# Optimization experiments

Measured on AMD Instinct MI355X. Metric: run time of the kernel, lower is better.

## Reference

```python
import jax, jax.numpy as jnp
import numpy as np

OFR = 2.0      # offset_range_factor
WSIZE = 8      # window_size
SPLIT = 1      # split_size


def _grid_sample(img, grid):
    # torch.nn.functional.grid_sample: bilinear, align_corners=True, padding_mode='zeros'
    # img: (B,C,H,W); grid: (B,Gh,Gw,2) with (x,y) in [-1,1]
    B, C, H, W = img.shape
    gx = (grid[..., 0] + 1.0) * 0.5 * (W - 1)
    gy = (grid[..., 1] + 1.0) * 0.5 * (H - 1)
    x0 = jnp.floor(gx)
    y0 = jnp.floor(gy)
    wx1 = gx - x0
    wy1 = gy - y0
    imgf = img.reshape(B, C, H * W)

    def corner(yc, xc, wgt):
        valid = (xc >= 0) & (xc <= W - 1) & (yc >= 0) & (yc <= H - 1)
        idx = (jnp.clip(yc, 0, H - 1) * W + jnp.clip(xc, 0, W - 1)).astype(jnp.int32)
        g = jnp.take_along_axis(imgf, idx.reshape(B, 1, -1), axis=2)  # (B,C,N)
        return g * (wgt * valid).reshape(B, 1, -1)

    out = (corner(y0, x0, (1 - wy1) * (1 - wx1)) + corner(y0, x0 + 1, (1 - wy1) * wx1)
           + corner(y0 + 1, x0, wy1 * (1 - wx1)) + corner(y0 + 1, x0 + 1, wy1 * wx1))
    return out.reshape(B, C, *grid.shape[1:-1])


def _win_attn(xqv, dh, dw):
    # 'b (qv c) (h dh) (w dw) -> qv (b h w) (dh dw) c' ; dot attention ; inverse rearrange
    B, cc, H, W = xqv.shape
    c = cc // 2
    t = xqv.reshape(B, 2, c, H // dh, dh, W // dw, dw)
    t = t.transpose(1, 0, 3, 5, 4, 6, 2).reshape(2, -1, dh * dw, c)
    q, v = t[0], t[1]
    atn = jax.nn.softmax(q @ jnp.swapaxes(q, -1, -2), axis=-1)
    o = atn @ v  # (nw, dh*dw, c)
    o = o.reshape(B, H // dh, W // dw, dh, dw, c).transpose(0, 5, 1, 3, 2, 4).reshape(B, c, H, W)
    return o


def setup_inputs() -> dict:
    key = jax.random.key(0)
    ks = jax.random.split(key, 16)
    C, B, H, W = 48, 2, 64, 64
    rn = lambda k, s, sc=0.05: (jax.random.normal(k, s) * sc).astype(jnp.float32)
    return {
        'x': jax.random.normal(ks[0], (B, C, H, W), jnp.float32),
        'Wq': rn(ks[1], (C, C)), 'bq': rn(ks[2], (C,)),
        'off_dw_w': rn(ks[3], (C, 1, 3, 3)), 'off_dw_b': rn(ks[4], (C,)),
        'off_ln_g': jnp.ones((C,), jnp.float32), 'off_ln_b': jnp.zeros((C,), jnp.float32),
        'off_pw_w': rn(ks[5], (2, C)),
        'Wk': rn(ks[6], (C, C)), 'bk': rn(ks[7], (C,)),
        'Wv': rn(ks[8], (C, C)), 'bv': rn(ks[9], (C,)),
        'inp_w': rn(ks[10], (2 * C, C)), 'inp_b': rn(ks[11], (2 * C,)),
        'bn_g': jnp.ones((2 * C,), jnp.float32), 'bn_b': jnp.zeros((2 * C,), jnp.float32),
        'bn_mean': jnp.zeros((2 * C,), jnp.float32), 'bn_var': jnp.ones((2 * C,), jnp.float32),
        'pout_w': rn(ks[12], (C, C)), 'pout_b': rn(ks[13], (C,)),
        'rpe': rn(ks[14], (1, 191, 191), 0.01),  # 96*2-1
    }


def reference(x, Wq, bq, off_dw_w, off_dw_b, off_ln_g, off_ln_b, off_pw_w, Wk, bk, Wv, bv,
              inp_w, inp_b, bn_g, bn_b, bn_mean, bn_var, pout_w, pout_b, rpe):
    B, C, h, w = x.shape
    scale = C ** (-0.5)
    c1 = lambda t, W_, b_=None: jnp.einsum('oc,bchw->bohw', W_, t) + (0.0 if b_ is None else b_[None, :, None, None])
    q = c1(x, Wq, bq)
    # conv_offset: depthwise 3x3 -> LayerNorm over channels -> GELU -> 1x1 to 2 ch (no bias)
    t = jax.lax.conv_general_dilated(q, off_dw_w, (1, 1), ((1, 1), (1, 1)),
                                     dimension_numbers=('NCHW', 'OIHW', 'NCHW'),
                                     feature_group_count=C) + off_dw_b[None, :, None, None]
    mu = t.mean(1, keepdims=True)
    var = ((t - mu) ** 2).mean(1, keepdims=True)
    t = (t - mu) * jax.lax.rsqrt(var + 1e-5) * off_ln_g[None, :, None, None] + off_ln_b[None, :, None, None]
    t = jax.nn.gelu(t, approximate=False)
    offset = c1(t, off_pw_w)  # (B,2,h,w), channel 0 = y, 1 = x
    n = h * w
    orange = jnp.array([1.0 / (h - 1), 1.0 / (w - 1)], jnp.float32).reshape(1, 2, 1, 1)
    offset = jnp.tanh(offset) * orange * OFR
    offset = offset.transpose(0, 2, 3, 1)  # (B,h,w,2) (y,x)
    ry = jnp.linspace(0.5, h - 0.5, h) / (h - 1) * 2.0 - 1.0
    rx = jnp.linspace(0.5, w - 0.5, w) / (w - 1) * 2.0 - 1.0
    ref = jnp.stack(jnp.meshgrid(ry, rx, indexing='ij'), -1)[None]
    pos = offset + ref  # (B,h,w,2) (y,x)
    x_sampled = _grid_sample(x, pos[..., ::-1]).reshape(B, C, n)
    # project_inp: 1x1 conv -> BatchNorm2d (eval mode)
    x2 = c1(x, inp_w, inp_b)
    x2 = (x2 - bn_mean[None, :, None, None]) * jax.lax.rsqrt(bn_var + 1e-5)[None, :, None, None] \
         * bn_g[None, :, None, None] + bn_b[None, :, None, None]
    s = 2 * C // 3
    xs0, xs1, xs2 = x2[:, :s], x2[:, s:2 * s], x2[:, 2 * s:]
    # deformable global attention
    qf = q.reshape(B, C, n)
    k = jnp.einsum('oc,bcn->bon', Wk, x_sampled) + bk[None, :, None]
    v = jnp.einsum('oc,bcn->bon', Wv, x_sampled) + bv[None, :, None]
    attn = jnp.einsum('bcm,bcn->bmn', qf, k) * scale
    gy = jnp.arange(h, dtype=jnp.float32) / (h - 1) * 2.0 - 1.0
    gx = jnp.arange(w, dtype=jnp.float32) / (w - 1) * 2.0 - 1.0
    qg = jnp.stack(jnp.meshgrid(gy, gx, indexing='ij'), -1).reshape(n, 2)
    disp = (qg[None, :, None, :] - pos.reshape(B, n, 2)[:, None, :, :]) * 0.5  # (B,m,n,2) (y,x)
    rpe_img = jnp.broadcast_to(rpe[None], (B,) + rpe.shape)  # (B,1,191,191)
    attn_bias = _grid_sample(rpe_img, disp[..., ::-1]).reshape(B, n, n)
    attn = jax.nn.softmax(attn + attn_bias, axis=2)
    out_dat = jnp.einsum('bmn,bcn->bcm', attn, v).reshape(B, C, h, w)
    # windowed / column / row local attention (shifts=0)
    out = jnp.concatenate([_win_attn(xs0, WSIZE, WSIZE),
                           _win_attn(xs1, h, SPLIT),
                           _win_attn(xs2, SPLIT, w)], axis=1)
    out = c1(out, pout_w, pout_b)
    return out * 0.5 + out_dat * 0.5
```

## Files before the change

kernel.cpp:

```cpp
#include <hip/hip_runtime.h>
#include <hip/hip_bf16.h>
#include <math.h>

#define Bsz 2
#define Cch 48
#define Hh 64
#define Ww 64
#define Nn 4096

typedef __bf16 bf16;
typedef __attribute__((ext_vector_type(8))) __bf16 bf16x8;
typedef __attribute__((ext_vector_type(4))) float f32x4;

__global__ void k_conv1x1(const float* __restrict__ in, const float* __restrict__ Wt,
                          const float* __restrict__ bias, float* __restrict__ qnc,
                          bf16* __restrict__ qbf){
  int chunk = blockIdx.x & 15;
  int o = (blockIdx.x >> 4) % Cch;
  int b = blockIdx.x / (16 * Cch);
  int p = chunk * 256 + threadIdx.x;
  float acc = bias[o];
  const float* ip = in + (b * Cch) * Nn + p;
  const float* wp = Wt + o * Cch;
  #pragma unroll
  for (int c = 0; c < Cch; c++) acc += wp[c] * ip[c * Nn];
  qnc[((size_t)(b * Nn + p)) * 48 + o] = acc;
  size_t qb = ((size_t)(b * Nn + p)) * 64;
  qbf[qb + o] = (bf16)acc;
  if (o < 16) qbf[qb + 48 + o] = (bf16)0.f;
}

__global__ __launch_bounds__(256) void k_offset_pos(const float* __restrict__ qnc,
                             const float* __restrict__ dww,
                             const float* __restrict__ dwb, const float* __restrict__ lng,
                             const float* __restrict__ lnb, const float* __restrict__ pww,
                             float* __restrict__ pos){
  int wv = threadIdx.x >> 6, lane = threadIdx.x & 63;
  int idx = blockIdx.x * 4 + wv;
  int b = idx >> 12;
  int p = idx & (Nn - 1);
  int y = p >> 6, x = p & 63;
  int c = lane;
  float t = 0.f;
  if (c < 48){
    t = dwb[c];
    #pragma unroll
    for (int ky = -1; ky <= 1; ky++){
      int yy = y + ky;
      if (yy < 0 || yy >= Hh) continue;
      #pragma unroll
      for (int kx = -1; kx <= 1; kx++){
        int xx = x + kx;
        if (xx < 0 || xx >= Ww) continue;
        t = fmaf(qnc[((size_t)(b * Nn + yy * Ww + xx)) * 48 + c],
                 dww[c * 9 + (ky + 1) * 3 + (kx + 1)], t);
      }
    }
  }
  float s = t;
  #pragma unroll
  for (int m = 1; m < 64; m <<= 1) s += __shfl_xor(s, m);
  float mean = s * (1.f / 48.f);
  float d = (c < 48) ? (t - mean) : 0.f;
  float v = d * d;
  #pragma unroll
  for (int m = 1; m < 64; m <<= 1) v += __shfl_xor(v, m);
  float rstd = rsqrtf(v * (1.f / 48.f) + 1e-5f);
  float p0 = 0.f, p1 = 0.f;
  if (c < 48){
    float u = (t - mean) * rstd * lng[c] + lnb[c];
    u = 0.5f * u * (1.f + erff(u * 0.70710678118654752f));
    p0 = pww[c] * u;
    p1 = pww[48 + c] * u;
  }
  #pragma unroll
  for (int m = 1; m < 64; m <<= 1){ p0 += __shfl_xor(p0, m); p1 += __shfl_xor(p1, m); }
  if (lane == 0){
    float posy = tanhf(p0) * (2.f / 63.f) + ((0.5f + (float)y) * (2.f / 63.f) - 1.f);
    float posx = tanhf(p1) * (2.f / 63.f) + ((0.5f + (float)x) * (2.f / 63.f) - 1.f);
    pos[idx * 2 + 0] = posy;
    pos[idx * 2 + 1] = posx;
  }
}

__global__ __launch_bounds__(512) void k_samplekv(const float* __restrict__ x,
                           const float* __restrict__ pos,
                           const float* __restrict__ Wk, const float* __restrict__ bk,
                           const float* __restrict__ Wv, const float* __restrict__ bv,
                           bf16* __restrict__ kk_bf, bf16* __restrict__ vt_bf,
                           float2* __restrict__ axay){
  __shared__ float wkt[48][49];
  __shared__ float wvt[48][49];
  __shared__ float rowb[8][48];
  int tid = threadIdx.x;
  for (int f = tid; f < 2304; f += 512){
    int o = f / 48, c = f - o * 48;
    wkt[c][o] = Wk[f];
    wvt[c][o] = Wv[f];
  }
  __syncthreads();
  int wv = tid >> 6, lane = tid & 63;
  int idx = blockIdx.x * 8 + wv;
  int b = idx >> 12;
  int n = idx & (Nn - 1);
  float py = pos[idx * 2], px = pos[idx * 2 + 1];
  if (lane == 0) axay[idx] = make_float2(95.f - 47.5f * py, 95.f - 47.5f * px);
  float gx = (px + 1.f) * 0.5f * 63.f;
  float gy = (py + 1.f) * 0.5f * 63.f;
  float x0f = floorf(gx), y0f = floorf(gy);
  float wx = gx - x0f, wy = gy - y0f;
  int x0 = (int)x0f, y0 = (int)y0f, x1 = x0 + 1, y1 = y0 + 1;
  float w00 = (1.f - wy) * (1.f - wx), w01 = (1.f - wy) * wx;
  float w10 = wy * (1.f - wx),         w11 = wy * wx;
  bool vx0 = (x0 >= 0) && (x0 < Ww), vx1 = (x1 >= 0) && (x1 < Ww);
  bool vy0 = (y0 >= 0) && (y0 < Hh), vy1 = (y1 >= 0) && (y1 < Hh);
  if (!(vx0 && vy0)) w00 = 0.f;
  if (!(vx1 && vy0)) w01 = 0.f;
  if (!(vx0 && vy1)) w10 = 0.f;
  if (!(vx1 && vy1)) w11 = 0.f;
  int cx0 = min(max(x0, 0), Ww - 1), cx1 = min(max(x1, 0), Ww - 1);
  int cy0 = min(max(y0, 0), Hh - 1), cy1 = min(max(y1, 0), Hh - 1);
  int i00 = cy0 * Ww + cx0, i01 = cy0 * Ww + cx1;
  int i10 = cy1 * Ww + cx0, i11 = cy1 * Ww + cx1;
  int c = lane;
  if (c < 48){
    const float* xc = x + ((size_t)(b * Cch + c)) * Nn;
    rowb[wv][c] = w00 * xc[i00] + w01 * xc[i01] + w10 * xc[i10] + w11 * xc[i11];
  }
  int o = lane;
  if (o < 48){
    float ka = bk[o], va = bv[o];
    #pragma unroll
    for (int cc = 0; cc < 48; cc++){
      float r = rowb[wv][cc];
      ka = fmaf(wkt[cc][o], r, ka);
      va = fmaf(wvt[cc][o], r, va);
    }
    kk_bf[(size_t)idx * 64 + o] = (bf16)ka;
    vt_bf[((size_t)(b * Cch + o)) * Nn + n] = (bf16)va;
  }
  if (o < 16) kk_bf[(size_t)idx * 64 + 48 + o] = (bf16)0.f;
}

__global__ __launch_bounds__(256, 4) void k_attn(const bf16* __restrict__ q_bf,
                                              const bf16* __restrict__ kk_bf,
                                              const bf16* __restrict__ vt_bf,
                                              const float2* __restrict__ axay,
                                              const float* __restrict__ rpe,
                                              float* __restrict__ o_part,
                                              float* __restrict__ s_part){
  __shared__ __align__(16) float g[128][26];
  __shared__ float axs[128], wy0s[128], wy1s[128];
  __shared__ int xlos[128], r0s[128], r1s[128];
  __shared__ __align__(16) bf16 ps[16][136];

  const int tid = threadIdx.x;
  const int b  = blockIdx.x >> 9;
  const int kp = (blockIdx.x >> 8) & 1;
  const int m0 = (blockIdx.x & 255) * 16;
  const int wid = tid >> 6, lane = tid & 63;
  const int q16 = lane >> 4, l16 = lane & 15;
  const int wn0 = wid * 32;

  const bf16* qb = q_bf + ((size_t)(b * Nn + m0 + l16)) * 64;
  bf16x8 qf0 = *(const bf16x8*)(qb + q16 * 8);
  bf16x8 qf1 = *(const bf16x8*)(qb + 32 + q16 * 8);

  const float qgy = (float)(m0 >> 6) * (2.f / 63.f) - 1.f;
  const float byq = 47.5f * qgy;
  const float scale = 0.14433756729740643f;
  const float bx0 = 47.5f * ((float)(m0 & 63) * (2.f / 63.f) - 1.f);
  float bxr[4];
  #pragma unroll
  for (int r = 0; r < 4; r++){
    int mcol = (m0 & 63) + q16 * 4 + r;
    bxr[r] = 47.5f * ((float)mcol * (2.f / 63.f) - 1.f);
  }

  f32x4 oacc[3];
  #pragma unroll
  for (int ct = 0; ct < 3; ct++) oacc[ct] = (f32x4){0.f, 0.f, 0.f, 0.f};
  float s_runw[4] = {0.f, 0.f, 0.f, 0.f};

  for (int chk = 0; chk < 16; chk++){
    const int n0 = kp * 2048 + chk * 128;
    if (lane < 32){
      int n = wn0 + lane;
      float2 aa = axay[(size_t)b * Nn + n0 + n];
      float gyr = aa.x + byq;
      float y0f = floorf(gyr);
      float wy = gyr - y0f;
      int y0 = (int)y0f, y1 = y0 + 1;
      wy0s[n] = ((unsigned)y0 < 191u) ? (1.f - wy) : 0.f;
      wy1s[n] = ((unsigned)y1 < 191u) ? wy : 0.f;
      r0s[n] = min(max(y0, 0), 190) * 191;
      r1s[n] = min(max(y1, 0), 190) * 191;
      axs[n] = aa.y;
      xlos[n] = (int)floorf(aa.y + bx0);
    }
    {
      int s = lane >> 5, jj = lane & 31;
      if (jj < 26){
        #pragma unroll
        for (int it = 0; it < 16; it++){
          int n = wn0 + it * 2 + s;
          int cx = min(max(xlos[n] + jj, 0), 190);
          g[n][jj] = wy0s[n] * rpe[r0s[n] + cx] + wy1s[n] * rpe[r1s[n] + cx];
        }
      }
    }
    f32x4 s0 = (f32x4){0.f, 0.f, 0.f, 0.f};
    f32x4 s1 = (f32x4){0.f, 0.f, 0.f, 0.f};
    {
      const bf16* kg = kk_bf + (size_t)(b * Nn + n0 + wn0 + l16) * 64;
      bf16x8 b00 = *(const bf16x8*)(kg + q16 * 8);
      bf16x8 b01 = *(const bf16x8*)(kg + 32 + q16 * 8);
      bf16x8 b10 = *(const bf16x8*)(kg + 16 * 64 + q16 * 8);
      bf16x8 b11 = *(const bf16x8*)(kg + 16 * 64 + 32 + q16 * 8);
      s0 = __builtin_amdgcn_mfma_f32_16x16x32_bf16(qf0, b00, s0, 0, 0, 0);
      s0 = __builtin_amdgcn_mfma_f32_16x16x32_bf16(qf1, b01, s0, 0, 0, 0);
      s1 = __builtin_amdgcn_mfma_f32_16x16x32_bf16(qf0, b10, s1, 0, 0, 0);
      s1 = __builtin_amdgcn_mfma_f32_16x16x32_bf16(qf1, b11, s1, 0, 0, 0);
    }
    float rs[4] = {0.f, 0.f, 0.f, 0.f};
    #pragma unroll
    for (int nt = 0; nt < 2; nt++){
      int nl = wn0 + nt * 16 + l16;
      float ax = axs[nl];
      int xb = xlos[nl];
      f32x4 sv = nt ? s1 : s0;
      #pragma unroll
      for (int r = 0; r < 4; r++){
        float gxr = ax + bxr[r];
        float x0f = floorf(gxr);
        float wx = gxr - x0f;
        int x0 = (int)x0f;
        float wx0 = ((unsigned)x0 < 191u) ? (1.f - wx) : 0.f;
        float wx1 = ((unsigned)(x0 + 1) < 191u) ? wx : 0.f;
        int j0 = min(max(x0 - xb, 0), 24);
        float bias = wx0 * g[nl][j0] + wx1 * g[nl][j0 + 1];
        float e = __expf(fmaf(sv[r], scale, bias));
        rs[r] += e;
        ps[q16 * 4 + r][nl] = (bf16)e;
      }
    }
    #pragma unroll
    for (int r = 0; r < 4; r++){
      float v = rs[r];
      #pragma unroll
      for (int msk = 1; msk < 16; msk <<= 1) v += __shfl_xor(v, msk);
      s_runw[r] += v;
    }
    {
      bf16x8 pa = *(const bf16x8*)&ps[l16][wn0 + q16 * 8];
      const bf16* vgb = vt_bf + (size_t)(b * Cch + l16) * Nn + n0 + wn0 + q16 * 8;
      #pragma unroll
      for (int ct = 0; ct < 3; ct++){
        bf16x8 vb = *(const bf16x8*)(vgb + (size_t)(ct * 16) * Nn);
        oacc[ct] = __builtin_amdgcn_mfma_f32_16x16x32_bf16(pa, vb, oacc[ct], 0, 0, 0);
      }
    }
  }
  __syncthreads();
  float* ored = (float*)g;
  float* sred = axs;
  #pragma unroll
  for (int ct = 0; ct < 3; ct++)
    #pragma unroll
    for (int r = 0; r < 4; r++)
      ored[(wid * 16 + q16 * 4 + r) * 48 + ct * 16 + l16] = oacc[ct][r];
  if (l16 == 0){
    #pragma unroll
    for (int r = 0; r < 4; r++) sred[wid * 16 + q16 * 4 + r] = s_runw[r];
  }
  __syncthreads();
  size_t obase = ((size_t)(b * 2 + kp) * Cch) * Nn;
  #pragma unroll
  for (int e = 0; e < 3; e++){
    int idx = tid + e * 256;
    int c = idx >> 4, mm = idx & 15;
    float v = ored[mm * 48 + c] + ored[(16 + mm) * 48 + c]
            + ored[(32 + mm) * 48 + c] + ored[(48 + mm) * 48 + c];
    o_part[obase + (size_t)c * Nn + m0 + mm] = v;
  }
  if (tid < 16)
    s_part[(size_t)(b * 2 + kp) * Nn + m0 + tid] =
        sred[tid] + sred[16 + tid] + sred[32 + tid] + sred[48 + tid];
}

__global__ __launch_bounds__(256) void k_win(const float* __restrict__ x,
                                             const float* __restrict__ iw,
                                             const float* __restrict__ ib,
                                             const float* __restrict__ bng,
                                             const float* __restrict__ bnb,
                                             const float* __restrict__ bnm,
                                             const float* __restrict__ bnv,
                                             float* __restrict__ wout){
  __shared__ __align__(16) bf16 xs[64][72];
  __shared__ __align__(16) bf16 wtt[32][72];
  __shared__ __align__(16) bf16 qs[64][72];
  __shared__ __align__(16) bf16 vst[16][72];
  __shared__ __align__(16) bf16 psw[64][72];
  __shared__ float bnsc[32], bnsh[32];
  int s = blockIdx.x >> 7;
  int r7 = blockIdx.x & 127;
  int b = r7 >> 6, wi = r7 & 63;
  int tid = threadIdx.x;
  int wid = tid >> 6, lane = tid & 63;
  int q16 = lane >> 4, l16 = lane & 15;
  for (int f = tid; f < 64 * 48; f += 256){
    int t = f & 63, c = f >> 6;
    int p = (s == 0) ? (((wi >> 3) * 8 + (t >> 3)) * 64 + (wi & 7) * 8 + (t & 7))
          : (s == 1) ? (t * 64 + wi) : (wi * 64 + t);
    xs[t][c] = (bf16)x[((size_t)(b * 48 + c)) * Nn + p];
  }
  for (int f = tid; f < 64 * 16; f += 256){
    int t = f >> 4, j = f & 15;
    xs[t][48 + j] = (bf16)0.f;
    qs[t][16 + j] = (bf16)0.f;
  }
  for (int f = tid; f < 32 * 64; f += 256){
    int o = f >> 6, c = f & 63;
    wtt[o][c] = (c < 48) ? (bf16)iw[(s * 32 + o) * 48 + c] : (bf16)0.f;
  }
  if (tid < 32){
    int ch = s * 32 + tid;
    float sc = bng[ch] * rsqrtf(bnv[ch] + 1e-5f);
    bnsc[tid] = sc;
    bnsh[tid] = (ib[ch] - bnm[ch]) * sc + bnb[ch];
  }
  __syncthreads();
  {
    bf16x8 a0 = *(const bf16x8*)&xs[wid * 16 + l16][q16 * 8];
    bf16x8 a1 = *(const bf16x8*)&xs[wid * 16 + l16][32 + q16 * 8];
    #pragma unroll
    for (int nt = 0; nt < 2; nt++){
      bf16x8 b0 = *(const bf16x8*)&wtt[nt * 16 + l16][q16 * 8];
      bf16x8 b1 = *(const bf16x8*)&wtt[nt * 16 + l16][32 + q16 * 8];
      f32x4 acc = (f32x4){0.f, 0.f, 0.f, 0.f};
      acc = __builtin_amdgcn_mfma_f32_16x16x32_bf16(a0, b0, acc, 0, 0, 0);
      acc = __builtin_amdgcn_mfma_f32_16x16x32_bf16(a1, b1, acc, 0, 0, 0);
      float scv = bnsc[nt * 16 + l16], shv = bnsh[nt * 16 + l16];
      #pragma unroll
      for (int r = 0; r < 4; r++){
        float v = fmaf(acc[r], scv, shv);
        int tok = wid * 16 + q16 * 4 + r;
        if (nt == 0) qs[tok][l16] = (bf16)v;
        else         vst[l16][tok] = (bf16)v;
      }
    }
  }
  __syncthreads();
  f32x4 sreg[4];
  {
    bf16x8 aq = *(const bf16x8*)&qs[wid * 16 + l16][q16 * 8];
    #pragma unroll
    for (int nt = 0; nt < 4; nt++){
      bf16x8 bq = *(const bf16x8*)&qs[nt * 16 + l16][q16 * 8];
      f32x4 acc = (f32x4){0.f, 0.f, 0.f, 0.f};
      sreg[nt] = __builtin_amdgcn_mfma_f32_16x16x32_bf16(aq, bq, acc, 0, 0, 0);
    }
  }
  float rinv[4];
  #pragma unroll
  for (int r = 0; r < 4; r++){
    float mx = fmaxf(fmaxf(sreg[0][r], sreg[1][r]), fmaxf(sreg[2][r], sreg[3][r]));
    #pragma unroll
    for (int msk = 1; msk < 16; msk <<= 1) mx = fmaxf(mx, __shfl_xor(mx, msk));
    float sum = 0.f;
    #pragma unroll
    for (int nt = 0; nt < 4; nt++){
      float e = __expf(sreg[nt][r] - mx);
      sum += e;
      psw[wid * 16 + q16 * 4 + r][nt * 16 + l16] = (bf16)e;
    }
    #pragma unroll
    for (int msk = 1; msk < 16; msk <<= 1) sum += __shfl_xor(sum, msk);
    rinv[r] = 1.f / sum;
  }
  f32x4 oac = (f32x4){0.f, 0.f, 0.f, 0.f};
  {
    bf16x8 pa0 = *(const bf16x8*)&psw[wid * 16 + l16][q16 * 8];
    bf16x8 pa1 = *(const bf16x8*)&psw[wid * 16 + l16][32 + q16 * 8];
    bf16x8 vb0 = *(const bf16x8*)&vst[l16][q16 * 8];
    bf16x8 vb1 = *(const bf16x8*)&vst[l16][32 + q16 * 8];
    oac = __builtin_amdgcn_mfma_f32_16x16x32_bf16(pa0, vb0, oac, 0, 0, 0);
    oac = __builtin_amdgcn_mfma_f32_16x16x32_bf16(pa1, vb1, oac, 0, 0, 0);
  }
  #pragma unroll
  for (int r = 0; r < 4; r++){
    int tok = wid * 16 + q16 * 4 + r;
    int p = (s == 0) ? (((wi >> 3) * 8 + (tok >> 3)) * 64 + (wi & 7) * 8 + (tok & 7))
          : (s == 1) ? (tok * 64 + wi) : (wi * 64 + tok);
    wout[((size_t)(b * 48 + s * 16 + l16)) * Nn + p] = oac[r] * rinv[r];
  }
}

__global__ void k_final(const float* __restrict__ win, const float* __restrict__ pw,
                        const float* __restrict__ pb, const float* __restrict__ o_part,
                        const float* __restrict__ s_part, float* __restrict__ out){
  int chunk = blockIdx.x & 15;
  int o = (blockIdx.x >> 4) % Cch;
  int b = blockIdx.x / (16 * Cch);
  int p = chunk * 256 + threadIdx.x;
  float acc = pb[o];
  const float* ip = win + (b * Cch) * Nn + p;
  const float* wp = pw + o * Cch;
  #pragma unroll
  for (int c = 0; c < Cch; c++) acc += wp[c] * ip[c * Nn];
  float sden = s_part[(size_t)(b * 2) * Nn + p] + s_part[(size_t)(b * 2 + 1) * Nn + p];
  float odv = (o_part[((size_t)(b * 2) * Cch + o) * Nn + p]
             + o_part[((size_t)(b * 2 + 1) * Cch + o) * Nn + p]) / sden;
  out[(b * Cch + o) * Nn + p] = 0.5f * acc + 0.5f * odv;
}

extern "C" void kernel_launch(void* const* d_in, const int* in_sizes, int n_in,
                              void* d_out, int out_size, void* d_ws, size_t ws_size,
                              hipStream_t stream){
  const float* x   = (const float*)d_in[0];
  const float* Wq  = (const float*)d_in[1];
  const float* bq  = (const float*)d_in[2];
  const float* dww = (const float*)d_in[3];
  const float* dwb = (const float*)d_in[4];
  const float* lng = (const float*)d_in[5];
  const float* lnb = (const float*)d_in[6];
  const float* pww = (const float*)d_in[7];
  const float* Wk  = (const float*)d_in[8];
  const float* bk  = (const float*)d_in[9];
  const float* Wv  = (const float*)d_in[10];
  const float* bv  = (const float*)d_in[11];
  const float* iw  = (const float*)d_in[12];
  const float* ib  = (const float*)d_in[13];
  const float* bng = (const float*)d_in[14];
  const float* bnb = (const float*)d_in[15];
  const float* bnm = (const float*)d_in[16];
  const float* bnv = (const float*)d_in[17];
  const float* pw  = (const float*)d_in[18];
  const float* pb  = (const float*)d_in[19];
  const float* rpe = (const float*)d_in[20];

  float*  ws     = (float*)d_ws;
  float*  qnc    = ws;
  float*  o_part = ws;
  float*  pos    = ws + 786432;
  float2* axay   = (float2*)(ws + 802816);
  float*  wout   = ws + 819200;
  bf16*   q_bf   = (bf16*)(ws + 1212416);
  bf16*   kk_bf  = (bf16*)(ws + 1474560);
  bf16*   vt_bf  = (bf16*)(ws + 1736704);
  float*  s_part = ws + 1933312;
  float*  out    = (float*)d_out;

  k_conv1x1   <<<Bsz * Cch * 16, 256, 0, stream>>>(x, Wq, bq, qnc, q_bf);
  k_offset_pos<<<(Bsz * Nn) / 4, 256, 0, stream>>>(qnc, dww, dwb, lng, lnb, pww, pos);
  k_samplekv  <<<(Bsz * Nn) / 8, 512, 0, stream>>>(x, pos, Wk, bk, Wv, bv,
                                                   kk_bf, vt_bf, axay);
  k_attn      <<<Bsz * 512, 256, 0, stream>>>(q_bf, kk_bf, vt_bf, axay, rpe,
                                              o_part, s_part);
  k_win       <<<384, 256, 0, stream>>>(x, iw, ib, bng, bnb, bnm, bnv, wout);
  k_final     <<<Bsz * Cch * 16, 256, 0, stream>>>(wout, pw, pb, o_part,
                                                   s_part, out);
}
```

Before: 206.4 us.

## Fuse global deformable attention and window attention into one launch, simplify bias sampling

Merges the deformable-attention kernel and the local window-attention kernel into a single launch: the first 1024 blocks do global attention and the remaining 384 do window attention, sharing one overlaid shared-memory buffer. It also bakes the x-boundary zeroing into the cached rpe rows so the inner bilinear bias becomes a single lerp, defers the per-row sum reduction to after the loop, and raises the launch-bounds occupancy hint from 4 to 5. The aim is to remove a launch and the tail gap between the two kernels, and to cut ALU work in the hot loop. The higher occupancy target may force register spills, and the unclamped j0 index relies on the g row covering every offset that occurs.

Result: faster. 199.6 us (-3.3%).

```diff
diff --git a/kernel.cpp b/kernel.cpp
--- a/kernel.cpp
+++ b/kernel.cpp
@@ -142,257 +142,262 @@
   if (o < 16) kk_bf[(size_t)idx * 64 + 48 + o] = (bf16)0.f;
 }
 
-__global__ __launch_bounds__(256, 4) void k_attn(const bf16* __restrict__ q_bf,
+__global__ __launch_bounds__(256, 5) void k_attn_win(const bf16* __restrict__ q_bf,
                                               const bf16* __restrict__ kk_bf,
                                               const bf16* __restrict__ vt_bf,
                                               const float2* __restrict__ axay,
                                               const float* __restrict__ rpe,
                                               float* __restrict__ o_part,
-                                              float* __restrict__ s_part){
-  __shared__ __align__(16) float g[128][26];
-  __shared__ float axs[128], wy0s[128], wy1s[128];
-  __shared__ int xlos[128], r0s[128], r1s[128];
-  __shared__ __align__(16) bf16 ps[16][136];
-
+                                              float* __restrict__ s_part,
+                                              const float* __restrict__ x,
+                                              const float* __restrict__ iw,
+                                              const float* __restrict__ ib,
+                                              const float* __restrict__ bng,
+                                              const float* __restrict__ bnb,
+                                              const float* __restrict__ bnm,
+                                              const float* __restrict__ bnv,
+                                              float* __restrict__ wout){
+  __shared__ __align__(16) char smem[25600];
   const int tid = threadIdx.x;
-  const int b  = blockIdx.x >> 9;
-  const int kp = (blockIdx.x >> 8) & 1;
-  const int m0 = (blockIdx.x & 255) * 16;
   const int wid = tid >> 6, lane = tid & 63;
   const int q16 = lane >> 4, l16 = lane & 15;
-  const int wn0 = wid * 32;
-
-  const bf16* qb = q_bf + ((size_t)(b * Nn + m0 + l16)) * 64;
-  bf16x8 qf0 = *(const bf16x8*)(qb + q16 * 8);
-  bf16x8 qf1 = *(const bf16x8*)(qb + 32 + q16 * 8);
-
-  const float qgy = (float)(m0 >> 6) * (2.f / 63.f) - 1.f;
-  const float byq = 47.5f * qgy;
-  const float scale = 0.14433756729740643f;
-  const float bx0 = 47.5f * ((float)(m0 & 63) * (2.f / 63.f) - 1.f);
-  float bxr[4];
-  #pragma unroll
-  for (int r = 0; r < 4; r++){
-    int mcol = (m0 & 63) + q16 * 4 + r;
-    bxr[r] = 47.5f * ((float)mcol * (2.f / 63.f) - 1.f);
-  }
-
-  f32x4 oacc[3];
-  #pragma unroll
-  for (int ct = 0; ct < 3; ct++) oacc[ct] = (f32x4){0.f, 0.f, 0.f, 0.f};
-  float s_runw[4] = {0.f, 0.f, 0.f, 0.f};
-
-  for (int chk = 0; chk < 16; chk++){
-    const int n0 = kp * 2048 + chk * 128;
-    if (lane < 32){
-      int n = wn0 + lane;
-      float2 aa = axay[(size_t)b * Nn + n0 + n];
-      float gyr = aa.x + byq;
-      float y0f = floorf(gyr);
-      float wy = gyr - y0f;
-      int y0 = (int)y0f, y1 = y0 + 1;
-      wy0s[n] = ((unsigned)y0 < 191u) ? (1.f - wy) : 0.f;
-      wy1s[n] = ((unsigned)y1 < 191u) ? wy : 0.f;
-      r0s[n] = min(max(y0, 0), 190) * 191;
-      r1s[n] = min(max(y1, 0), 190) * 191;
-      axs[n] = aa.y;
-      xlos[n] = (int)floorf(aa.y + bx0);
-    }
+
+  if (blockIdx.x < 1024){
+    float (*g)[26] = (float(*)[26])smem;
+    float* axs  = (float*)(smem + 13312);
+    int*   xlos = (int*)  (smem + 13824);
+    float* wy0s = (float*)(smem + 14336);
+    float* wy1s = (float*)(smem + 14848);
+    int*   r0s  = (int*)  (smem + 15360);
+    int*   r1s  = (int*)  (smem + 15872);
+    bf16 (*ps)[136] = (bf16(*)[136])(smem + 16384);
+
+    const int b  = blockIdx.x >> 9;
+    const int kp = (blockIdx.x >> 8) & 1;
+    const int m0 = (blockIdx.x & 255) * 16;
+    const int wn0 = wid * 32;
+
+    const bf16* qb = q_bf + ((size_t)(b * Nn + m0 + l16)) * 64;
+    bf16x8 qf0 = *(const bf16x8*)(qb + q16 * 8);
+    bf16x8 qf1 = *(const bf16x8*)(qb + 32 + q16 * 8);
+
+    const float qgy = (float)(m0 >> 6) * (2.f / 63.f) - 1.f;
+    const float byq = 47.5f * qgy;
+    const float scale = 0.14433756729740643f;
+    const float bx0 = 47.5f * ((float)(m0 & 63) * (2.f / 63.f) - 1.f);
+    float bxr[4];
+    #pragma unroll
+    for (int r = 0; r < 4; r++){
+      int mcol = (m0 & 63) + q16 * 4 + r;
+      bxr[r] = 47.5f * ((float)mcol * (2.f / 63.f) - 1.f);
+    }
+
+    f32x4 oacc[3];
+    #pragma unroll
+    for (int ct = 0; ct < 3; ct++) oacc[ct] = (f32x4){0.f, 0.f, 0.f, 0.f};
+    float s_runw[4] = {0.f, 0.f, 0.f, 0.f};
+
+    for (int chk = 0; chk < 16; chk++){
+      const int n0 = kp * 2048 + chk * 128;
+      if (lane < 32){
+        int n = wn0 + lane;
+        float2 aa = axay[(size_t)b * Nn + n0 + n];
+        float gyr = aa.x + byq;
+        float y0f = floorf(gyr);
+        float wy = gyr - y0f;
+        int y0 = (int)y0f, y1 = y0 + 1;
+        wy0s[n] = ((unsigned)y0 < 191u) ? (1.f - wy) : 0.f;
+        wy1s[n] = ((unsigned)y1 < 191u) ? wy : 0.f;
+        r0s[n] = min(max(y0, 0), 190) * 191;
+        r1s[n] = min(max(y1, 0), 190) * 191;
+        axs[n] = aa.y;
+        xlos[n] = (int)floorf(aa.y + bx0);
+      }
+      {
+        int s = lane >> 5, jj = lane & 31;
+        if (jj < 26){
+          #pragma unroll
+          for (int it = 0; it < 16; it++){
+            int n = wn0 + it * 2 + s;
+            int xg = xlos[n] + jj;
+            int cx = min(max(xg, 0), 190);
+            float val = wy0s[n] * rpe[r0s[n] + cx] + wy1s[n] * rpe[r1s[n] + cx];
+            g[n][jj] = ((unsigned)xg < 191u) ? val : 0.f;
+          }
+        }
+      }
+      f32x4 s0 = (f32x4){0.f, 0.f, 0.f, 0.f};
+      f32x4 s1 = (f32x4){0.f, 0.f, 0.f, 0.f};
+      {
+        const bf16* kg = kk_bf + (size_t)(b * Nn + n0 + wn0 + l16) * 64;
+        bf16x8 b00 = *(const bf16x8*)(kg + q16 * 8);
+        bf16x8 b01 = *(const bf16x8*)(kg + 32 + q16 * 8);
+        bf16x8 b10 = *(const bf16x8*)(kg + 16 * 64 + q16 * 8);
+        bf16x8 b11 = *(const bf16x8*)(kg + 16 * 64 + 32 + q16 * 8);
+        s0 = __builtin_amdgcn_mfma_f32_16x16x32_bf16(qf0, b00, s0, 0, 0, 0);
+        s0 = __builtin_amdgcn_mfma_f32_16x16x32_bf16(qf1, b01, s0, 0, 0, 0);
+        s1 = __builtin_amdgcn_mfma_f32_16x16x32_bf16(qf0, b10, s1, 0, 0, 0);
+        s1 = __builtin_amdgcn_mfma_f32_16x16x32_bf16(qf1, b11, s1, 0, 0, 0);
+      }
+      #pragma unroll
+      for (int nt = 0; nt < 2; nt++){
+        int nl = wn0 + nt * 16 + l16;
+        float ax = axs[nl];
+        int xb = xlos[nl];
+        f32x4 sv = nt ? s1 : s0;
+        #pragma unroll
+        for (int r = 0; r < 4; r++){
+          float gxr = ax + bxr[r];
+          float x0f = floorf(gxr);
+          float wx = gxr - x0f;
+          int j0 = (int)x0f - xb;
+          float g0 = g[nl][j0], g1 = g[nl][j0 + 1];
+          float bias = fmaf(wx, g1 - g0, g0);
+          float e = __expf(fmaf(sv[r], scale, bias));
+          s_runw[r] += e;
+          ps[q16 * 4 + r][nl] = (bf16)e;
+        }
+      }
+      {
+        bf16x8 pa = *(const bf16x8*)&ps[l16][wn0 + q16 * 8];
+        const bf16* vgb = vt_bf + (size_t)(b * Cch + l16) * Nn + n0 + wn0 + q16 * 8;
+        #pragma unroll
+        for (int ct = 0; ct < 3; ct++){
+          bf16x8 vb = *(const bf16x8*)(vgb + (size_t)(ct * 16) * Nn);
+          oacc[ct] = __builtin_amdgcn_mfma_f32_16x16x32_bf16(pa, vb, oacc[ct], 0, 0, 0);
+        }
+      }
+    }
+    #pragma unroll
+    for (int r = 0; r < 4; r++){
+      #pragma unroll
+      for (int msk = 1; msk < 16; msk <<= 1)
+        s_runw[r] += __shfl_xor(s_runw[r], msk);
+    }
+    __syncthreads();
+    float* ored = (float*)g;
+    float* sred = axs;
+    #pragma unroll
+    for (int ct = 0; ct < 3; ct++)
+      #pragma unroll
+      for (int r = 0; r < 4; r++)
+        ored[(wid * 16 + q16 * 4 + r) * 48 + ct * 16 + l16] = oacc[ct][r];
+    if (l16 == 0){
+      #pragma unroll
+      for (int r = 0; r < 4; r++) sred[wid * 16 + q16 * 4 + r] = s_runw[r];
+    }
+    __syncthreads();
+    size_t obase = ((size_t)(b * 2 + kp) * Cch) * Nn;
+    #pragma unroll
+    for (int e = 0; e < 3; e++){
+      int idx = tid + e * 256;
+      int c = idx >> 4, mm = idx & 15;
+      float v = ored[mm * 48 + c] + ored[(16 + mm) * 48 + c]
+              + ored[(32 + mm) * 48 + c] + ored[(48 + mm) * 48 + c];
+      o_part[obase + (size_t)c * Nn + m0 + mm] = v;
+    }
+    if (tid < 16)
+      s_part[(size_t)(b * 2 + kp) * Nn + m0 + tid] =
+          sred[tid] + sred[16 + tid] + sred[32 + tid] + sred[48 + tid];
+  } else {
+    bf16 (*xs)[72]  = (bf16(*)[72])smem;
+    bf16 (*wtt)[72] = (bf16(*)[72])(smem + 9216);
+    bf16 (*qs)[72]  = (bf16(*)[72])(smem + 13824);
+    bf16 (*vst)[72] = (bf16(*)[72])(smem + 23040);
+    float* bnsc = (float*)(smem + 25344);
+    float* bnsh = (float*)(smem + 25472);
+    bf16 (*psw)[72] = xs;
+
+    int wb = blockIdx.x - 1024;
+    int s = wb >> 7;
+    int r7 = wb & 127;
+    int b = r7 >> 6, wi = r7 & 63;
+    for (int f = tid; f < 64 * 48; f += 256){
+      int t = f & 63, c = f >> 6;
+      int p = (s == 0) ? (((wi >> 3) * 8 + (t >> 3)) * 64 + (wi & 7) * 8 + (t & 7))
+            : (s == 1) ? (t * 64 + wi) : (wi * 64 + t);
+      xs[t][c] = (bf16)x[((size_t)(b * 48 + c)) * Nn + p];
+    }
+    for (int f = tid; f < 64 * 16; f += 256){
+      int t = f >> 4, j = f & 15;
+      xs[t][48 + j] = (bf16)0.f;
+      qs[t][16 + j] = (bf16)0.f;
+    }
+    for (int f = tid; f < 32 * 64; f += 256){
+      int o = f >> 6, c = f & 63;
+      wtt[o][c] = (c < 48) ? (bf16)iw[(s * 32 + o) * 48 + c] : (bf16)0.f;
+    }
+    if (tid < 32){
+      int ch = s * 32 + tid;
+      float sc = bng[ch] * rsqrtf(bnv[ch] + 1e-5f);
+      bnsc[tid] = sc;
+      bnsh[tid] = (ib[ch] - bnm[ch]) * sc + bnb[ch];
+    }
+    __syncthreads();
     {
-      int s = lane >> 5, jj = lane & 31;
-      if (jj < 26){
+      bf16x8 a0 = *(const bf16x8*)&xs[wid * 16 + l16][q16 * 8];
+      bf16x8 a1 = *(const bf16x8*)&xs[wid * 16 + l16][32 + q16 * 8];
+      #pragma unroll
+      for (int nt = 0; nt < 2; nt++){
+        bf16x8 b0 = *(const bf16x8*)&wtt[nt * 16 + l16][q16 * 8];
+        bf16x8 b1 = *(const bf16x8*)&wtt[nt * 16 + l16][32 + q16 * 8];
+        f32x4 acc = (f32x4){0.f, 0.f, 0.f, 0.f};
+        acc = __builtin_amdgcn_mfma_f32_16x16x32_bf16(a0, b0, acc, 0, 0, 0);
+        acc = __builtin_amdgcn_mfma_f32_16x16x32_bf16(a1, b1, acc, 0, 0, 0);
+        float scv = bnsc[nt * 16 + l16], shv = bnsh[nt * 16 + l16];
         #pragma unroll
-        for (int it = 0; it < 16; it++){
-          int n = wn0 + it * 2 + s;
-          int cx = min(max(xlos[n] + jj, 0), 190);
-          g[n][jj] = wy0s[n] * rpe[r0s[n] + cx] + wy1s[n] * rpe[r1s[n] + cx];
+        for (int r = 0; r < 4; r++){
+          float v = fmaf(acc[r], scv, shv);
+          int tok = wid * 16 + q16 * 4 + r;
+          if (nt == 0) qs[tok][l16] = (bf16)v;
+          else         vst[l16][tok] = (bf16)v;
         }
       }
     }
-    f32x4 s0 = (f32x4){0.f, 0.f, 0.f, 0.f};
-    f32x4 s1 = (f32x4){0.f, 0.f, 0.f, 0.f};
+    __syncthreads();
+    f32x4 sreg[4];
     {
-      const bf16* kg = kk_bf + (size_t)(b * Nn + n0 + wn0 + l16) * 64;
-      bf16x8 b00 = *(const bf16x8*)(kg + q16 * 8);
-      bf16x8 b01 = *(const bf16x8*)(kg + 32 + q16 * 8);
-      bf16x8 b10 = *(const bf16x8*)(kg + 16 * 64 + q16 * 8);
-      bf16x8 b11 = *(const bf16x8*)(kg + 16 * 64 + 32 + q16 * 8);
-      s0 = __builtin_amdgcn_mfma_f32_16x16x32_bf16(qf0, b00, s0, 0, 0, 0);
-      s0 = __builtin_amdgcn_mfma_f32_16x16x32_bf16(qf1, b01, s0, 0, 0, 0);
-      s1 = __builtin_amdgcn_mfma_f32_16x16x32_bf16(qf0, b10, s1, 0, 0, 0);
-      s1 = __builtin_amdgcn_mfma_f32_16x16x32_bf16(qf1, b11, s1, 0, 0, 0);
-    }
-    float rs[4] = {0.f, 0.f, 0.f, 0.f};
-    #pragma unroll
-    for (int nt = 0; nt < 2; nt++){
-      int nl = wn0 + nt * 16 + l16;
-      float ax = axs[nl];
-      int xb = xlos[nl];
-      f32x4 sv = nt ? s1 : s0;
-      #pragma unroll
-      for (int r = 0; r < 4; r++){
-        float gxr = ax + bxr[r];
-        float x0f = floorf(gxr);
-        float wx = gxr - x0f;
-        int x0 = (int)x0f;
-        float wx0 = ((unsigned)x0 < 191u) ? (1.f - wx) : 0.f;
-        float wx1 = ((unsigned)(x0 + 1) < 191u) ? wx : 0.f;
-        int j0 = min(max(x0 - xb, 0), 24);
-        float bias = wx0 * g[nl][j0] + wx1 * g[nl][j0 + 1];
-        float e = __expf(fmaf(sv[r], scale, bias));
-        rs[r] += e;
-        ps[q16 * 4 + r][nl] = (bf16)e;
-      }
-    }
+      bf16x8 aq = *(const bf16x8*)&qs[wid * 16 + l16][q16 * 8];
+      #pragma unroll
+      for (int nt = 0; nt < 4; nt++){
+        bf16x8 bq = *(const bf16x8*)&qs[nt * 16 + l16][q16 * 8];
+        f32x4 acc = (f32x4){0.f, 0.f, 0.f, 0.f};
+        sreg[nt] = __builtin_amdgcn_mfma_f32_16x16x32_bf16(aq, bq, acc, 0, 0, 0);
+      }
+    }
+    float rinv[4];
     #pragma unroll
     for (int r = 0; r < 4; r++){
-      float v = rs[r];
-      #pragma unroll
-      for (int msk = 1; msk < 16; msk <<= 1) v += __shfl_xor(v, msk);
-      s_runw[r] += v;
-    }
+      float mx = fmaxf(fmaxf(sreg[0][r], sreg[1][r]), fmaxf(sreg[2][r], sreg[3][r]));
+      #pragma unroll
+      for (int msk = 1; msk < 16; msk <<= 1) mx = fmaxf(mx, __shfl_xor(mx, msk));
+      float sum = 0.f;
+      #pragma unroll
+      for (int nt = 0; nt < 4; nt++){
+        float e = __expf(sreg[nt][r] - mx);
+        sum += e;
+        psw[wid * 16 + q16 * 4 + r][nt * 16 + l16] = (bf16)e;
+      }
+      #pragma unroll
+      for (int msk = 1; msk < 16; msk <<= 1) sum += __shfl_xor(sum, msk);
+      rinv[r] = 1.f / sum;
+    }
+    f32x4 oac = (f32x4){0.f, 0.f, 0.f, 0.f};
     {
-      bf16x8 pa = *(const bf16x8*)&ps[l16][wn0 + q16 * 8];
-      const bf16* vgb = vt_bf + (size_t)(b * Cch + l16) * Nn + n0 + wn0 + q16 * 8;
-      #pragma unroll
-      for (int ct = 0; ct < 3; ct++){
-        bf16x8 vb = *(const bf16x8*)(vgb + (size_t)(ct * 16) * Nn);
-        oacc[ct] = __builtin_amdgcn_mfma_f32_16x16x32_bf16(pa, vb, oacc[ct], 0, 0, 0);
-      }
-    }
-  }
-  __syncthreads();
-  float* ored = (float*)g;
-  float* sred = axs;
-  #pragma unroll
-  for (int ct = 0; ct < 3; ct++)
-    #pragma unroll
-    for (int r = 0; r < 4; r++)
-      ored[(wid * 16 + q16 * 4 + r) * 48 + ct * 16 + l16] = oacc[ct][r];
-  if (l16 == 0){
-    #pragma unroll
-    for (int r = 0; r < 4; r++) sred[wid * 16 + q16 * 4 + r] = s_runw[r];
-  }
-  __syncthreads();
-  size_t obase = ((size_t)(b * 2 + kp) * Cch) * Nn;
-  #pragma unroll
-  for (int e = 0; e < 3; e++){
-    int idx = tid + e * 256;
-    int c = idx >> 4, mm = idx & 15;
-    float v = ored[mm * 48 + c] + ored[(16 + mm) * 48 + c]
-            + ored[(32 + mm) * 48 + c] + ored[(48 + mm) * 48 + c];
-    o_part[obase + (size_t)c * Nn + m0 + mm] = v;
-  }
-  if (tid < 16)
-    s_part[(size_t)(b * 2 + kp) * Nn + m0 + tid] =
-        sred[tid] + sred[16 + tid] + sred[32 + tid] + sred[48 + tid];
-}
-
-__global__ __launch_bounds__(256) void k_win(const float* __restrict__ x,
-                                             const float* __restrict__ iw,
-                                             const float* __restrict__ ib,
-                                             const float* __restrict__ bng,
-                                             const float* __restrict__ bnb,
-                                             const float* __restrict__ bnm,
-                                             const float* __restrict__ bnv,
-                                             float* __restrict__ wout){
-  __shared__ __align__(16) bf16 xs[64][72];
-  __shared__ __align__(16) bf16 wtt[32][72];
-  __shared__ __align__(16) bf16 qs[64][72];
-  __shared__ __align__(16) bf16 vst[16][72];
-  __shared__ __align__(16) bf16 psw[64][72];
-  __shared__ float bnsc[32], bnsh[32];
-  int s = blockIdx.x >> 7;
-  int r7 = blockIdx.x & 127;
-  int b = r7 >> 6, wi = r7 & 63;
-  int tid = threadIdx.x;
-  int wid = tid >> 6, lane = tid & 63;
-  int q16 = lane >> 4, l16 = lane & 15;
-  for (int f = tid; f < 64 * 48; f += 256){
-    int t = f & 63, c = f >> 6;
-    int p = (s == 0) ? (((wi >> 3) * 8 + (t >> 3)) * 64 + (wi & 7) * 8 + (t & 7))
-          : (s == 1) ? (t * 64 + wi) : (wi * 64 + t);
-    xs[t][c] = (bf16)x[((size_t)(b * 48 + c)) * Nn + p];
-  }
-  for (int f = tid; f < 64 * 16; f += 256){
-    int t = f >> 4, j = f & 15;
-    xs[t][48 + j] = (bf16)0.f;
-    qs[t][16 + j] = (bf16)0.f;
-  }
-  for (int f = tid; f < 32 * 64; f += 256){
-    int o = f >> 6, c = f & 63;
-    wtt[o][c] = (c < 48) ? (bf16)iw[(s * 32 + o) * 48 + c] : (bf16)0.f;
-  }
-  if (tid < 32){
-    int ch = s * 32 + tid;
-    float sc = bng[ch] * rsqrtf(bnv[ch] + 1e-5f);
-    bnsc[tid] = sc;
-    bnsh[tid] = (ib[ch] - bnm[ch]) * sc + bnb[ch];
-  }
-  __syncthreads();
-  {
-    bf16x8 a0 = *(const bf16x8*)&xs[wid * 16 + l16][q16 * 8];
-    bf16x8 a1 = *(const bf16x8*)&xs[wid * 16 + l16][32 + q16 * 8];
-    #pragma unroll
-    for (int nt = 0; nt < 2; nt++){
-      bf16x8 b0 = *(const bf16x8*)&wtt[nt * 16 + l16][q16 * 8];
-      bf16x8 b1 = *(const bf16x8*)&wtt[nt * 16 + l16][32 + q16 * 8];
-      f32x4 acc = (f32x4){0.f, 0.f, 0.f, 0.f};
-      acc = __builtin_amdgcn_mfma_f32_16x16x32_bf16(a0, b0, acc, 0, 0, 0);
-      acc = __builtin_amdgcn_mfma_f32_16x16x32_bf16(a1, b1, acc, 0, 0, 0);
-      float scv = bnsc[nt * 16 + l16], shv = bnsh[nt * 16 + l16];
-      #pragma unroll
-      for (int r = 0; r < 4; r++){
-        float v = fmaf(acc[r], scv, shv);
-        int tok = wid * 16 + q16 * 4 + r;
-        if (nt == 0) qs[tok][l16] = (bf16)v;
-        else         vst[l16][tok] = (bf16)v;
-      }
-    }
-  }
-  __syncthreads();
-  f32x4 sreg[4];
-  {
-    bf16x8 aq = *(const bf16x8*)&qs[wid * 16 + l16][q16 * 8];
-    #pragma unroll
-    for (int nt = 0; nt < 4; nt++){
-      bf16x8 bq = *(const bf16x8*)&qs[nt * 16 + l16][q16 * 8];
-      f32x4 acc = (f32x4){0.f, 0.f, 0.f, 0.f};
-      sreg[nt] = __builtin_amdgcn_mfma_f32_16x16x32_bf16(aq, bq, acc, 0, 0, 0);
-    }
-  }
-  float rinv[4];
-  #pragma unroll
-  for (int r = 0; r < 4; r++){
-    float mx = fmaxf(fmaxf(sreg[0][r], sreg[1][r]), fmaxf(sreg[2][r], sreg[3][r]));
-    #pragma unroll
-    for (int msk = 1; msk < 16; msk <<= 1) mx = fmaxf(mx, __shfl_xor(mx, msk));
-    float sum = 0.f;
-    #pragma unroll
-    for (int nt = 0; nt < 4; nt++){
-      float e = __expf(sreg[nt][r] - mx);
-      sum += e;
-      psw[wid * 16 + q16 * 4 + r][nt * 16 + l16] = (bf16)e;
-    }
-    #pragma unroll
-    for (int msk = 1; msk < 16; msk <<= 1) sum += __shfl_xor(sum, msk);
-    rinv[r] = 1.f / sum;
-  }
-  f32x4 oac = (f32x4){0.f, 0.f, 0.f, 0.f};
-  {
-    bf16x8 pa0 = *(const bf16x8*)&psw[wid * 16 + l16][q16 * 8];
-    bf16x8 pa1 = *(const bf16x8*)&psw[wid * 16 + l16][32 + q16 * 8];
-    bf16x8 vb0 = *(const bf16x8*)&vst[l16][q16 * 8];
-    bf16x8 vb1 = *(const bf16x8*)&vst[l16][32 + q16 * 8];
-    oac = __builtin_amdgcn_mfma_f32_16x16x32_bf16(pa0, vb0, oac, 0, 0, 0);
-    oac = __builtin_amdgcn_mfma_f32_16x16x32_bf16(pa1, vb1, oac, 0, 0, 0);
-  }
-  #pragma unroll
-  for (int r = 0; r < 4; r++){
-    int tok = wid * 16 + q16 * 4 + r;
-    int p = (s == 0) ? (((wi >> 3) * 8 + (tok >> 3)) * 64 + (wi & 7) * 8 + (tok & 7))
-          : (s == 1) ? (tok * 64 + wi) : (wi * 64 + tok);
-    wout[((size_t)(b * 48 + s * 16 + l16)) * Nn + p] = oac[r] * rinv[r];
+      bf16x8 pa0 = *(const bf16x8*)&psw[wid * 16 + l16][q16 * 8];
+      bf16x8 pa1 = *(const bf16x8*)&psw[wid * 16 + l16][32 + q16 * 8];
+      bf16x8 vb0 = *(const bf16x8*)&vst[l16][q16 * 8];
+      bf16x8 vb1 = *(const bf16x8*)&vst[l16][32 + q16 * 8];
+      oac = __builtin_amdgcn_mfma_f32_16x16x32_bf16(pa0, vb0, oac, 0, 0, 0);
+      oac = __builtin_amdgcn_mfma_f32_16x16x32_bf16(pa1, vb1, oac, 0, 0, 0);
+    }
+    #pragma unroll
+    for (int r = 0; r < 4; r++){
+      int tok = wid * 16 + q16 * 4 + r;
+      int p = (s == 0) ? (((wi >> 3) * 8 + (tok >> 3)) * 64 + (wi & 7) * 8 + (tok & 7))
+            : (s == 1) ? (tok * 64 + wi) : (wi * 64 + tok);
+      wout[((size_t)(b * 48 + s * 16 + l16)) * Nn + p] = oac[r] * rinv[r];
+    }
   }
 }
 
@@ -455,9 +460,9 @@
   k_offset_pos<<<(Bsz * Nn) / 4, 256, 0, stream>>>(qnc, dww, dwb, lng, lnb, pww, pos);
   k_samplekv  <<<(Bsz * Nn) / 8, 512, 0, stream>>>(x, pos, Wk, bk, Wv, bv,
                                                    kk_bf, vt_bf, axay);
-  k_attn      <<<Bsz * 512, 256, 0, stream>>>(q_bf, kk_bf, vt_bf, axay, rpe,
-                                              o_part, s_part);
-  k_win       <<<384, 256, 0, stream>>>(x, iw, ib, bng, bnb, bnm, bnv, wout);
+  k_attn_win  <<<Bsz * 512 + 384, 256, 0, stream>>>(q_bf, kk_bf, vt_bf, axay, rpe,
+                                                    o_part, s_part,
+                                                    x, iw, ib, bng, bnb, bnm, bnv, wout);
   k_final     <<<Bsz * Cch * 16, 256, 0, stream>>>(wout, pw, pb, o_part,
                                                    s_part, out);
 }
```
